# Performance work log

Measured on AMD Instinct MI355X. Metric: run time of the kernel, lower is better.

Reference implementation:

```python
import jax, jax.numpy as jnp
import numpy as np
from jax import lax

RADIUS = 0.2
K = 32
EPS = 1e-5  # torch BatchNorm default eps

B, N, M, C = 16, 4096, 1024, 64


def setup_inputs() -> dict:
    key = jax.random.key(0)
    ks = jax.random.split(key, 8)
    src_x = jax.random.normal(ks[0], (B, N, C), dtype=jnp.float32)
    src_xyz = jax.random.uniform(ks[1], (B, N, 3), dtype=jnp.float32)
    xyz = jax.random.uniform(ks[2], (B, M, 3), dtype=jnp.float32)
    w1 = jax.random.normal(ks[3], (64, C + 3), dtype=jnp.float32) * 0.05
    w2 = jax.random.normal(ks[4], (128, 64), dtype=jnp.float32) * 0.05
    w3 = jax.random.normal(ks[5], (256, 128), dtype=jnp.float32) * 0.05
    return {
        "src_x": src_x, "src_xyz": src_xyz, "xyz": xyz,
        "w1": w1, "g1": jnp.ones(64), "b1": jnp.zeros(64),
        "w2": w2, "g2": jnp.ones(128), "b2": jnp.zeros(128),
        "w3": w3, "gl": jnp.ones(256), "bl": jnp.zeros(256),
    }


def _ball_query(src_xyz, xyz):
    # squared distances [B, M, N]
    d2 = jnp.sum((xyz[:, :, None, :] - src_xyz[:, None, :, :]) ** 2, axis=-1)
    n = src_xyz.shape[1]
    col = jnp.arange(n, dtype=jnp.int32)
    # encode: in-ball points keep their index, others get sentinel n
    score = jnp.where(d2 <= RADIUS * RADIUS, col, n)
    neg_top, _ = lax.top_k(-score, K)        # k smallest scores (first-k in index order)
    gidx = -neg_top                          # [B, M, K]
    first = gidx[..., :1]
    first = jnp.where(first >= n, 0, first)  # no neighbor at all -> 0 (degenerate)
    gidx = jnp.where(gidx >= n, first, gidx)  # pad slots repeat first neighbor
    return gidx


def _gather(src, gidx):
    # src [B, N, D], gidx [B, M, K] -> [B, M, K, D]
    b, m, k = gidx.shape
    out = jnp.take_along_axis(src, gidx.reshape(b, m * k, 1), axis=1)
    return out.reshape(b, m, k, src.shape[-1])


def _bn(x, g, b, axes):
    # training-mode batch norm over given axes, per last-dim channel (biased var)
    mean = jnp.mean(x, axis=axes, keepdims=True)
    var = jnp.mean((x - mean) ** 2, axis=axes, keepdims=True)
    return (x - mean) * lax.rsqrt(var + EPS) * g + b


def _gelu(x):
    return jax.nn.gelu(x, approximate=False)  # torch nn.GELU default (erf)


def reference(src_x, src_xyz, xyz, w1, g1, b1, w2, g2, b2, w3, gl, bl):
    gidx = _ball_query(src_xyz, xyz)                 # [B, M, K]
    grouped_xyz = _gather(src_xyz, gidx)             # [B, M, K, 3]
    centered = grouped_xyz - xyz[:, :, None, :]
    grouped_x = _gather(src_x, gidx)                 # [B, M, K, C]
    feat = jnp.concatenate([centered, grouped_x], axis=-1)  # [B, M, K, C+3]

    h = _gelu(_bn(jnp.einsum("bmkc,oc->bmko", feat, w1), g1, b1, (0, 1, 2)))
    h = _gelu(_bn(jnp.einsum("bmkc,oc->bmko", h, w2), g2, b2, (0, 1, 2)))
    h = jnp.einsum("bmkc,oc->bmko", h, w3)
    h = jnp.max(h, axis=2)                           # max over k neighbors -> [B, M, 256]
    return _gelu(_bn(h, gl, bl, (0, 1)))             # BatchNorm1d over (batch, points)
```

## Files before the change

kernel.cpp:

```cpp
#include <hip/hip_runtime.h>
#include <math.h>

#define BB 16
#define NN 4096
#define MM 1024
#define KNN 32
#define R2 0.04f
#define EPSV 1e-5f
#define S1f ((float)(BB * MM * KNN))
#define S3f ((float)(BB * MM))

typedef __attribute__((ext_vector_type(8))) short short8;
typedef __attribute__((ext_vector_type(4))) short short4v;
typedef __attribute__((ext_vector_type(4))) float f32x4;

__device__ __forceinline__ short f2b(float x) {
    union { float f; unsigned u; } v; v.f = x;
    unsigned r = v.u + 0x7fffu + ((v.u >> 16) & 1u);
    return (short)(r >> 16);
}
__device__ __forceinline__ float b2f(short s) {
    union { unsigned u; float f; } v; v.u = ((unsigned)(unsigned short)s) << 16;
    return v.f;
}
__device__ __forceinline__ float gelu_t(float x) {
    float u = 0.7978845608f * x * (1.f + 0.044715f * x * x);
    float e = __expf(2.f * u);
    float r = __builtin_amdgcn_rcpf(e + 1.f);
    return x - x * r;
}
__device__ __forceinline__ float gelu_e(float x) {
    return 0.5f * x * (1.f + erff(x * 0.7071067811865475f));
}
__device__ __forceinline__ f32x4 zero4() { f32x4 z = {0.f, 0.f, 0.f, 0.f}; return z; }
__device__ __forceinline__ f32x4 mfma(short8 a, short8 b, f32x4 c) {
    return __builtin_amdgcn_mfma_f32_16x16x32_bf16(a, b, c, 0, 0, 0);
}
__device__ __forceinline__ short8 pack8(f32x4 a, f32x4 b) {
    short8 r;
    r[0] = f2b(a[0]); r[1] = f2b(a[1]); r[2] = f2b(a[2]); r[3] = f2b(a[3]);
    r[4] = f2b(b[0]); r[5] = f2b(b[1]); r[6] = f2b(b[2]); r[7] = f2b(b[3]);
    return r;
}

__global__ __launch_bounds__(256) void k_ballquery(const float* __restrict__ src_xyz,
                                                   const float* __restrict__ xyz,
                                                   int* __restrict__ gidx) {
    __shared__ float sx[NN], sy[NN], sz[NN];
    int t = threadIdx.x;
    int lane = t & 63, w = t >> 6;
    int q0 = blockIdx.x * 16;
    int b = q0 >> 10;
    const float* sp = src_xyz + (size_t)b * NN * 3;
    for (int i = t; i < NN * 3; i += 256) {
        float v = sp[i];
        int j = i / 3, d = i - j * 3;
        if (d == 0) sx[j] = v;
        else if (d == 1) sy[j] = v;
        else sz[j] = v;
    }
    __syncthreads();
#pragma unroll
    for (int qi = 0; qi < 4; ++qi) {
        int q = q0 + w * 4 + qi;
        int m = q & 1023;
        float qx = xyz[((size_t)b * MM + m) * 3 + 0];
        float qy = xyz[((size_t)b * MM + m) * 3 + 1];
        float qz = xyz[((size_t)b * MM + m) * 3 + 2];
        int* outp = gidx + (size_t)q * KNN;
        int cnt = 0, firstj = -1;
        for (int j0 = 0; j0 < NN && cnt < KNN; j0 += 64) {
            int j = j0 + lane;
            float dx = qx - sx[j];
            float dy = qy - sy[j];
            float dz = qz - sz[j];
            bool hit = (dx * dx + dy * dy + dz * dz) <= R2;
            unsigned long long mask = __ballot(hit);
            if (hit) {
                int rank = cnt + __popcll(mask & ((1ull << lane) - 1ull));
                if (rank < KNN) outp[rank] = j;
            }
            if (firstj < 0 && mask != 0ull) firstj = j0 + __ffsll((long long)mask) - 1;
            cnt += __popcll(mask);
        }
        if (cnt < KNN) {
            int fj = (firstj < 0) ? 0 : firstj;
            for (int k = cnt + lane; k < KNN; k += 64) outp[k] = fj;
        }
    }
}

__global__ __launch_bounds__(256) void k_prep(const float* __restrict__ src_x,
                                              const float* __restrict__ w1,
                                              const float* __restrict__ w2,
                                              const float* __restrict__ w3,
                                              short* __restrict__ src_xb,
                                              short* __restrict__ w1p,
                                              short* __restrict__ w2p,
                                              short* __restrict__ w3p) {
    int i = blockIdx.x * 256 + threadIdx.x;
    if (i < 524288) {
        const f32x4* p = (const f32x4*)(src_x + (size_t)i * 8);
        *(short8*)(src_xb + (size_t)i * 8) = pack8(p[0], p[1]);
    } else {
        int j = i - 524288;
        if (j < 6144) {
            int e = j & 7, lane = (j >> 3) & 63, idx = j >> 9;
            int kf = idx >> 2, nf = idx & 3;
            int ln = lane & 15, qq = lane >> 4;
            int n = nf * 16 + ln, k = kf * 32 + qq * 8 + e;
            float v = 0.f;
            if (k < 64) v = w1[n * 67 + 3 + k];
            else if (k < 67) v = w1[n * 67 + (k - 64)];
            w1p[j] = f2b(v);
        } else if (j < 14336) {
            int j2 = j - 6144;
            int e = j2 & 7, lane = (j2 >> 3) & 63, idx = j2 >> 9;
            int kf = idx >> 3, nf = idx & 7;
            int ln = lane & 15, qq = lane >> 4;
            w2p[j2] = f2b(w2[(nf * 16 + ln) * 64 + kf * 32 + qq * 8 + e]);
        } else if (j < 47104) {
            int j2 = j - 14336;
            int e = j2 & 7, lane = (j2 >> 3) & 63, idx = j2 >> 9;
            int nf = idx & 3, kf = (idx >> 2) & 3, nc = idx >> 4;
            int ln = lane & 15, qq = lane >> 4;
            w3p[j2] = f2b(w3[(size_t)(nc * 64 + nf * 16 + ln) * 128 + kf * 32 + qq * 8 + e]);
        }
    }
}

#define GATHER_WAVE(R)                                                                  \
    {                                                                                   \
        if (lane < 8) { short4v z4 = {0, 0, 0, 0};                                      \
            *(short4v*)((R) + 2304 + lane * 4) = z4; }                                  \
        int r = lane >> 1, hf = lane & 1;                                               \
        int jdx = gidx[(size_t)g * KNN + r];                                            \
        const short8* sp = (const short8*)(src_xb + ((size_t)b * NN + jdx) * 64 + hf * 32); \
        *(short8*)((R) + r * 72 + hf * 32) = sp[0];                                     \
        *(short8*)((R) + r * 72 + hf * 32 + 8) = sp[1];                                 \
        *(short8*)((R) + r * 72 + hf * 32 + 16) = sp[2];                                \
        *(short8*)((R) + r * 72 + hf * 32 + 24) = sp[3];                                \
        if (hf == 0) {                                                                  \
            const float* spp = src_xyz + ((size_t)b * NN + jdx) * 3;                    \
            short4v z;                                                                  \
            z[0] = f2b(spp[0] - qx); z[1] = f2b(spp[1] - qy);                           \
            z[2] = f2b(spp[2] - qz); z[3] = 0;                                          \
            *(short4v*)((R) + r * 72 + 64) = z;                                         \
            short4v z0 = {0, 0, 0, 0};                                                  \
            *(short4v*)((R) + r * 72 + 68) = z0;                                        \
        }                                                                               \
    }

#define BN1_SCALES                                                                      \
    if (t < 64) {                                                                       \
        float s = 0.f, sq = 0.f;                                                        \
        _Pragma("unroll")                                                               \
        for (int r = 0; r < 8; ++r) { s += stats1[r * 128 + t]; sq += stats1[r * 128 + 64 + t]; } \
        float mu = s * (1.f / S1f);                                                     \
        float var = sq * (1.f / S1f) - mu * mu;                                         \
        float rs = rsqrtf(var + EPSV);                                                  \
        float sc = g1[t] * rs;                                                          \
        sc1L[t] = sc;                                                                   \
        sh1L[t] = b1[t] - mu * sc;                                                      \
    }

#define L1_SWAPPED(R, acc1)                                                             \
    short8 bAct[2][3];                                                                  \
    _Pragma("unroll")                                                                   \
    for (int sf = 0; sf < 2; ++sf)                                                      \
        _Pragma("unroll")                                                               \
        for (int kf = 0; kf < 3; ++kf)                                                  \
            bAct[sf][kf] = *(const short8*)((R) + (sf * 16 + ln) * 72 + kf * 32 + qq * 8); \
    _Pragma("unroll")                                                                   \
    for (int sf = 0; sf < 2; ++sf)                                                      \
        _Pragma("unroll")                                                               \
        for (int nf = 0; nf < 4; ++nf) acc1[sf][nf] = zero4();                          \
    _Pragma("unroll")                                                                   \
    for (int kf = 0; kf < 3; ++kf)                                                      \
        _Pragma("unroll")                                                               \
        for (int nf = 0; nf < 4; ++nf) {                                                \
            short8 aW = *(const short8*)(w1p + (((kf * 4 + nf) * 64) + lane) * 8);      \
            acc1[0][nf] = mfma(aW, bAct[0][kf], acc1[0][nf]);                           \
            acc1[1][nf] = mfma(aW, bAct[1][kf], acc1[1][nf]);                           \
        }

__global__ __launch_bounds__(256, 6) void k_s1(const int* __restrict__ gidx,
                                               const float* __restrict__ src_xyz,
                                               const float* __restrict__ xyz,
                                               const short* __restrict__ src_xb,
                                               const short* __restrict__ w1p,
                                               float* __restrict__ stats1) {
    __shared__ short wbuf[4][2336];
    __shared__ float redS[256], redQ[256];
    int t = threadIdx.x, lane = t & 63, w = t >> 6, ln = lane & 15, qq = lane >> 4;
    int g = blockIdx.x * 4 + w, b = g >> 10, m = g & 1023;
    float qx = xyz[((size_t)b * MM + m) * 3 + 0];
    float qy = xyz[((size_t)b * MM + m) * 3 + 1];
    float qz = xyz[((size_t)b * MM + m) * 3 + 2];
    short* R = wbuf[w];
    GATHER_WAVE(R)
    short8 aAct[2][3];
#pragma unroll
    for (int sf = 0; sf < 2; ++sf)
#pragma unroll
        for (int kf = 0; kf < 3; ++kf)
            aAct[sf][kf] = *(const short8*)(R + (sf * 16 + ln) * 72 + kf * 32 + qq * 8);
    f32x4 acc1[2][4];
#pragma unroll
    for (int sf = 0; sf < 2; ++sf)
#pragma unroll
        for (int nf = 0; nf < 4; ++nf) acc1[sf][nf] = zero4();
#pragma unroll
    for (int kf = 0; kf < 3; ++kf)
#pragma unroll
        for (int nf = 0; nf < 4; ++nf) {
            short8 bW = *(const short8*)(w1p + (((kf * 4 + nf) * 64) + lane) * 8);
            acc1[0][nf] = mfma(aAct[0][kf], bW, acc1[0][nf]);
            acc1[1][nf] = mfma(aAct[1][kf], bW, acc1[1][nf]);
        }
#pragma unroll
    for (int nf = 0; nf < 4; ++nf) {
        f32x4 sv, qv;
#pragma unroll
        for (int jj = 0; jj < 4; ++jj) {
            float a0 = acc1[0][nf][jj], a1 = acc1[1][nf][jj];
            sv[jj] = a0 + a1; qv[jj] = a0 * a0 + a1 * a1;
        }
        float s = (sv[0] + sv[1]) + (sv[2] + sv[3]);
        float q = (qv[0] + qv[1]) + (qv[2] + qv[3]);
        s += __shfl_xor(s, 16); s += __shfl_xor(s, 32);
        q += __shfl_xor(q, 16); q += __shfl_xor(q, 32);
        if (qq == 0) { redS[w * 64 + nf * 16 + ln] = s; redQ[w * 64 + nf * 16 + ln] = q; }
    }
    __syncthreads();
    if (t < 64) {
        float s = redS[t] + redS[64 + t] + redS[128 + t] + redS[192 + t];
        float q = redQ[t] + redQ[64 + t] + redQ[128 + t] + redQ[192 + t];
        float* st = stats1 + (blockIdx.x & 7) * 128;
        atomicAdd(&st[t], s);
        atomicAdd(&st[64 + t], q);
    }
}

__global__ __launch_bounds__(256, 4) void k_s2(const int* __restrict__ gidx,
                                               const float* __restrict__ src_xyz,
                                               const float* __restrict__ xyz,
                                               const short* __restrict__ src_xb,
                                               const short* __restrict__ w1p,
                                               const short* __restrict__ w2p,
                                               const float* __restrict__ g1,
                                               const float* __restrict__ b1,
                                               const float* __restrict__ stats1,
                                               float* __restrict__ stats2,
                                               short* __restrict__ h2p) {
    __shared__ short wbuf[4][2336];
    __shared__ float sc1L[64], sh1L[64];
    __shared__ float redS[512], redQ[512];
    int t = threadIdx.x, lane = t & 63, w = t >> 6, ln = lane & 15, qq = lane >> 4;
    int g = blockIdx.x * 4 + w, b = g >> 10, m = g & 1023;
    float qx = xyz[((size_t)b * MM + m) * 3 + 0];
    float qy = xyz[((size_t)b * MM + m) * 3 + 1];
    float qz = xyz[((size_t)b * MM + m) * 3 + 2];
    short* R = wbuf[w];
    GATHER_WAVE(R)
    BN1_SCALES
    f32x4 acc1[2][4];
    L1_SWAPPED(R, acc1)
    __syncthreads();
#pragma unroll
    for (int sf = 0; sf < 2; ++sf)
#pragma unroll
        for (int nf = 0; nf < 4; ++nf) {
            int c0 = nf * 16 + qq * 4;
            f32x4 sc = *(const f32x4*)(sc1L + c0);
            f32x4 sh = *(const f32x4*)(sh1L + c0);
            short4v sv;
#pragma unroll
            for (int jj = 0; jj < 4; ++jj)
                sv[jj] = f2b(gelu_t(acc1[sf][nf][jj] * sc[jj] + sh[jj]));
            *(short4v*)(R + (sf * 16 + ln) * 72 + c0) = sv;
        }
    short8 bh1[2][2];
#pragma unroll
    for (int sf = 0; sf < 2; ++sf)
#pragma unroll
        for (int kf = 0; kf < 2; ++kf)
            bh1[sf][kf] = *(const short8*)(R + (sf * 16 + ln) * 72 + kf * 32 + qq * 8);
    f32x4 acc2[2][8];
#pragma unroll
    for (int sf = 0; sf < 2; ++sf)
#pragma unroll
        for (int nf = 0; nf < 8; ++nf) acc2[sf][nf] = zero4();
#pragma unroll
    for (int kf = 0; kf < 2; ++kf)
#pragma unroll
        for (int nf = 0; nf < 8; ++nf) {
            short8 aW = *(const short8*)(w2p + (((kf * 8 + nf) * 64) + lane) * 8);
            acc2[0][nf] = mfma(aW, bh1[0][kf], acc2[0][nf]);
            acc2[1][nf] = mfma(aW, bh1[1][kf], acc2[1][nf]);
        }
    {
        short* hb2 = h2p + (size_t)g * 4096;
#pragma unroll
        for (int i = 0; i < 8; ++i) {
            int sf = i >> 2, p = i & 3;
            *(short8*)(hb2 + (i * 64 + lane) * 8) = pack8(acc2[sf][2 * p], acc2[sf][2 * p + 1]);
        }
    }
#pragma unroll
    for (int nf = 0; nf < 8; ++nf) {
        f32x4 s, q;
#pragma unroll
        for (int jj = 0; jj < 4; ++jj) {
            float a0 = acc2[0][nf][jj], a1 = acc2[1][nf][jj];
            s[jj] = a0 + a1; q[jj] = a0 * a0 + a1 * a1;
        }
#pragma unroll
        for (int d = 1; d < 16; d <<= 1) {
#pragma unroll
            for (int jj = 0; jj < 4; ++jj) {
                s[jj] += __shfl_xor(s[jj], d);
                q[jj] += __shfl_xor(q[jj], d);
            }
        }
        if (ln == 0) {
            *(f32x4*)(redS + w * 128 + nf * 16 + qq * 4) = s;
            *(f32x4*)(redQ + w * 128 + nf * 16 + qq * 4) = q;
        }
    }
    __syncthreads();
    if (t < 128) {
        float s = redS[t] + redS[128 + t] + redS[256 + t] + redS[384 + t];
        float q = redQ[t] + redQ[128 + t] + redQ[256 + t] + redQ[384 + t];
        float* st = stats2 + (blockIdx.x & 7) * 256;
        atomicAdd(&st[t], s);
        atomicAdd(&st[128 + t], q);
    }
}

__global__ __launch_bounds__(256, 4) void k3(const short* __restrict__ h2p,
                                             const short* __restrict__ w3p,
                                             const float* __restrict__ g2,
                                             const float* __restrict__ b2,
                                             const float* __restrict__ stats2,
                                             float* __restrict__ stats3,
                                             float* __restrict__ out) {
    __shared__ short wbuf[4][4352];
    __shared__ float sc2L[128], sh2L[128];
    __shared__ float mxS[4][256];
    int t = threadIdx.x, lane = t & 63, w = t >> 6, ln = lane & 15, qq = lane >> 4;
    int g = blockIdx.x * 4 + w;
    const short* hb = h2p + (size_t)g * 4096;
    short8 hv[8];
#pragma unroll
    for (int i = 0; i < 8; ++i) hv[i] = *(const short8*)(hb + (i * 64 + lane) * 8);
    if (t < 128) {
        float s = 0.f, sq = 0.f;
#pragma unroll
        for (int r = 0; r < 8; ++r) { s += stats2[r * 256 + t]; sq += stats2[r * 256 + 128 + t]; }
        float mu = s * (1.f / S1f);
        float var = sq * (1.f / S1f) - mu * mu;
        float rs = rsqrtf(var + EPSV);
        float sc = g2[t] * rs;
        sc2L[t] = sc;
        sh2L[t] = b2[t] - mu * sc;
    }
    __syncthreads();
    short* R = wbuf[w];
#pragma unroll
    for (int i = 0; i < 8; ++i) {
        int sf = i >> 2, p = i & 3;
#pragma unroll
        for (int hh = 0; hh < 2; ++hh) {
            int c0 = (2 * p + hh) * 16 + qq * 4;
            f32x4 sc = *(const f32x4*)(sc2L + c0);
            f32x4 sh = *(const f32x4*)(sh2L + c0);
            short4v sv;
#pragma unroll
            for (int jj = 0; jj < 4; ++jj)
                sv[jj] = f2b(gelu_t(b2f(hv[i][hh * 4 + jj]) * sc[jj] + sh[jj]));
            *(short4v*)(R + (sf * 16 + ln) * 136 + c0) = sv;
        }
    }
    short8 a3[2][4];
#pragma unroll
    for (int sf = 0; sf < 2; ++sf)
#pragma unroll
        for (int kf = 0; kf < 4; ++kf)
            a3[sf][kf] = *(const short8*)(R + (sf * 16 + ln) * 136 + kf * 32 + qq * 8);
#pragma unroll
    for (int nc = 0; nc < 4; ++nc) {
        f32x4 acc3[2][4];
#pragma unroll
        for (int sf = 0; sf < 2; ++sf)
#pragma unroll
            for (int nf = 0; nf < 4; ++nf) acc3[sf][nf] = zero4();
#pragma unroll
        for (int kf = 0; kf < 4; ++kf)
#pragma unroll
            for (int nf = 0; nf < 4; ++nf) {
                short8 bW = *(const short8*)(w3p + (((nc * 4 + kf) * 4 + nf) * 64 + lane) * 8);
                acc3[0][nf] = mfma(a3[0][kf], bW, acc3[0][nf]);
                acc3[1][nf] = mfma(a3[1][kf], bW, acc3[1][nf]);
            }
#pragma unroll
        for (int nf = 0; nf < 4; ++nf) {
            f32x4 v0 = acc3[0][nf], v1 = acc3[1][nf];
            float m0 = fmaxf(fmaxf(v0[0], v0[1]), fmaxf(v0[2], v0[3]));
            float m1 = fmaxf(fmaxf(v1[0], v1[1]), fmaxf(v1[2], v1[3]));
            float mm = fmaxf(m0, m1);
            mm = fmaxf(mm, __shfl_xor(mm, 16));
            mm = fmaxf(mm, __shfl_xor(mm, 32));
            if (qq == 0) {
                out[(size_t)g * 256 + nc * 64 + nf * 16 + ln] = mm;
                mxS[w][nc * 64 + nf * 16 + ln] = mm;
            }
        }
    }
    __syncthreads();
    {
        float a0 = mxS[0][t], a1 = mxS[1][t], a2 = mxS[2][t], a3v = mxS[3][t];
        float s = a0 + a1 + a2 + a3v;
        float q = a0 * a0 + a1 * a1 + a2 * a2 + a3v * a3v;
        float* st = stats3 + (blockIdx.x & 7) * 512;
        atomicAdd(&st[t], s);
        atomicAdd(&st[256 + t], q);
    }
}

__global__ __launch_bounds__(256) void k_bn3(float* __restrict__ out,
                                             const float* __restrict__ stats3,
                                             const float* __restrict__ gl,
                                             const float* __restrict__ bl) {
    int i = blockIdx.x * 256 + threadIdx.x;
    int o = i & 255;
    float s = 0.f, q = 0.f;
#pragma unroll
    for (int r = 0; r < 8; ++r) { s += stats3[r * 512 + o]; q += stats3[r * 512 + 256 + o]; }
    float mu = s * (1.f / S3f);
    float var = q * (1.f / S3f) - mu * mu;
    float rs = rsqrtf(var + EPSV);
    float x = out[i];
    out[i] = gelu_e((x - mu) * rs * gl[o] + bl[o]);
}

extern "C" void kernel_launch(void* const* d_in, const int* in_sizes, int n_in,
                              void* d_out, int out_size, void* d_ws, size_t ws_size,
                              hipStream_t stream) {
    const float* src_x   = (const float*)d_in[0];
    const float* src_xyz = (const float*)d_in[1];
    const float* xyz     = (const float*)d_in[2];
    const float* w1      = (const float*)d_in[3];
    const float* g1      = (const float*)d_in[4];
    const float* b1      = (const float*)d_in[5];
    const float* w2      = (const float*)d_in[6];
    const float* g2      = (const float*)d_in[7];
    const float* b2      = (const float*)d_in[8];
    const float* w3      = (const float*)d_in[9];
    const float* gl      = (const float*)d_in[10];
    const float* bl      = (const float*)d_in[11];
    float* out = (float*)d_out;

    int* gidx = (int*)d_ws;
    float* statsF = (float*)(gidx + BB * MM * KNN);
    float* stats1 = statsF;
    float* stats2 = statsF + 1024;
    float* stats3 = statsF + 3072;
    short* wb = (short*)(statsF + 7168);
    short* w1p = wb;
    short* w2p = wb + 6144;
    short* w3p = wb + 14336;
    short* src_xb = wb + 47104;
    short* h2p = (short*)((char*)d_ws + (size_t)(16u << 20));

    hipMemsetAsync(statsF, 0, 7168 * sizeof(float), stream);
    k_prep<<<2232, 256, 0, stream>>>(src_x, w1, w2, w3, src_xb, w1p, w2p, w3p);
    k_ballquery<<<(BB * MM) / 16, 256, 0, stream>>>(src_xyz, xyz, gidx);
    k_s1<<<(BB * MM) / 4, 256, 0, stream>>>(gidx, src_xyz, xyz, src_xb, w1p, stats1);
    k_s2<<<(BB * MM) / 4, 256, 0, stream>>>(gidx, src_xyz, xyz, src_xb, w1p, w2p, g1, b1,
                                            stats1, stats2, h2p);
    k3<<<(BB * MM) / 4, 256, 0, stream>>>(h2p, w3p, g2, b2, stats2, stats3, out);
    k_bn3<<<BB * MM, 256, 0, stream>>>(out, stats3, gl, bl);
}
```

Baseline: 229.2 us.

## Store h2 in MFMA operand layout so k3 skips LDS transpose

k_s2 now transposes its layer-2 output through shared memory and writes h2 to global in the A-operand fragment layout k3 consumes. k3 can then apply BN2 and GELU directly in registers and feed MFMA without a shared-memory staging buffer. Dropping k3's LDS buffer lets it raise its launch-bounds occupancy hint from 4 to 6. In exchange, k_s2 gets a larger shared buffer and an extra LDS round trip, which may lower its occupancy.

```diff
diff --git a/kernel.cpp b/kernel.cpp
--- a/kernel.cpp
+++ b/kernel.cpp
@@ -253,7 +253,7 @@
                                                const float* __restrict__ stats1,
                                                float* __restrict__ stats2,
                                                short* __restrict__ h2p) {
-    __shared__ short wbuf[4][2336];
+    __shared__ short wbuf[4][4352];
     __shared__ float sc1L[64], sh1L[64];
     __shared__ float redS[512], redQ[512];
     int t = threadIdx.x, lane = t & 63, w = t >> 6, ln = lane & 15, qq = lane >> 4;
@@ -299,13 +299,26 @@
             acc2[0][nf] = mfma(aW, bh1[0][kf], acc2[0][nf]);
             acc2[1][nf] = mfma(aW, bh1[1][kf], acc2[1][nf]);
         }
+#pragma unroll
+    for (int sf = 0; sf < 2; ++sf)
+#pragma unroll
+        for (int nf = 0; nf < 8; ++nf) {
+            int c0 = nf * 16 + qq * 4;
+            short4v sv;
+#pragma unroll
+            for (int jj = 0; jj < 4; ++jj)
+                sv[jj] = f2b(acc2[sf][nf][jj]);
+            *(short4v*)(R + (sf * 16 + ln) * 136 + c0) = sv;
+        }
     {
         short* hb2 = h2p + (size_t)g * 4096;
 #pragma unroll
-        for (int i = 0; i < 8; ++i) {
-            int sf = i >> 2, p = i & 3;
-            *(short8*)(hb2 + (i * 64 + lane) * 8) = pack8(acc2[sf][2 * p], acc2[sf][2 * p + 1]);
-        }
+        for (int sf = 0; sf < 2; ++sf)
+#pragma unroll
+            for (int kf = 0; kf < 4; ++kf) {
+                short8 fr = *(const short8*)(R + (sf * 16 + ln) * 136 + kf * 32 + qq * 8);
+                *(short8*)(hb2 + ((sf * 4 + kf) * 64 + lane) * 8) = fr;
+            }
     }
 #pragma unroll
     for (int nf = 0; nf < 8; ++nf) {
@@ -338,22 +351,24 @@
     }
 }
 
-__global__ __launch_bounds__(256, 4) void k3(const short* __restrict__ h2p,
+__global__ __launch_bounds__(256, 6) void k3(const short* __restrict__ h2p,
                                              const short* __restrict__ w3p,
                                              const float* __restrict__ g2,
                                              const float* __restrict__ b2,
                                              const float* __restrict__ stats2,
                                              float* __restrict__ stats3,
                                              float* __restrict__ out) {
-    __shared__ short wbuf[4][4352];
     __shared__ float sc2L[128], sh2L[128];
     __shared__ float mxS[4][256];
     int t = threadIdx.x, lane = t & 63, w = t >> 6, ln = lane & 15, qq = lane >> 4;
     int g = blockIdx.x * 4 + w;
-    const short* hb = h2p + (size_t)g * 4096;
-    short8 hv[8];
-#pragma unroll
-    for (int i = 0; i < 8; ++i) hv[i] = *(const short8*)(hb + (i * 64 + lane) * 8);
+    const short* hbp = h2p + (size_t)g * 4096;
+    short8 hv[2][4];
+#pragma unroll
+    for (int sf = 0; sf < 2; ++sf)
+#pragma unroll
+        for (int kf = 0; kf < 4; ++kf)
+            hv[sf][kf] = *(const short8*)(hbp + ((sf * 4 + kf) * 64 + lane) * 8);
     if (t < 128) {
         float s = 0.f, sq = 0.f;
 #pragma unroll
@@ -366,28 +381,26 @@
         sh2L[t] = b2[t] - mu * sc;
     }
     __syncthreads();
-    short* R = wbuf[w];
-#pragma unroll
-    for (int i = 0; i < 8; ++i) {
-        int sf = i >> 2, p = i & 3;
-#pragma unroll
-        for (int hh = 0; hh < 2; ++hh) {
-            int c0 = (2 * p + hh) * 16 + qq * 4;
-            f32x4 sc = *(const f32x4*)(sc2L + c0);
-            f32x4 sh = *(const f32x4*)(sh2L + c0);
-            short4v sv;
-#pragma unroll
-            for (int jj = 0; jj < 4; ++jj)
-                sv[jj] = f2b(gelu_t(b2f(hv[i][hh * 4 + jj]) * sc[jj] + sh[jj]));
-            *(short4v*)(R + (sf * 16 + ln) * 136 + c0) = sv;
-        }
-    }
     short8 a3[2][4];
 #pragma unroll
     for (int sf = 0; sf < 2; ++sf)
 #pragma unroll
-        for (int kf = 0; kf < 4; ++kf)
-            a3[sf][kf] = *(const short8*)(R + (sf * 16 + ln) * 136 + kf * 32 + qq * 8);
+        for (int kf = 0; kf < 4; ++kf) {
+            int c0 = kf * 32 + qq * 8;
+            f32x4 sa = *(const f32x4*)(sc2L + c0);
+            f32x4 sb = *(const f32x4*)(sc2L + c0 + 4);
+            f32x4 ha = *(const f32x4*)(sh2L + c0);
+            f32x4 hbv = *(const f32x4*)(sh2L + c0 + 4);
+            short8 r = hv[sf][kf];
+            short8 o;
+#pragma unroll
+            for (int e = 0; e < 4; ++e)
+                o[e] = f2b(gelu_t(b2f(r[e]) * sa[e] + ha[e]));
+#pragma unroll
+            for (int e = 0; e < 4; ++e)
+                o[e + 4] = f2b(gelu_t(b2f(r[e + 4]) * sb[e] + hbv[e]));
+            a3[sf][kf] = o;
+        }
 #pragma unroll
     for (int nc = 0; nc < 4; ++nc) {
         f32x4 acc3[2][4];
```

Result: slower. 287.7 us (+25.5%).
